# Kernel tuning notes

Measured on AMD Instinct MI355X. Metric: run time of the kernel, lower is better.

Reference implementation:

```python
import jax, jax.numpy as jnp
import numpy as np
from jax import lax

B, S, T = 4096, 4096, 2  # batch, seq_length, num_tags (CRF(2) hardcoded in ToNySegmenter)


def setup_inputs() -> dict:
    key = jax.random.key(0)
    k_em, k_st, k_en, k_tr, k_tg, k_len = jax.random.split(key, 6)
    emissions = jax.random.normal(k_em, (B, S, T), dtype=jnp.float32)
    start_transitions = jax.random.uniform(k_st, (T,), dtype=jnp.float32, minval=-1.0, maxval=1.0)
    end_transitions = jax.random.uniform(k_en, (T,), dtype=jnp.float32, minval=-1.0, maxval=1.0)
    transitions = jax.random.uniform(k_tr, (T, T), dtype=jnp.float32, minval=-1.0, maxval=1.0)
    tags = jax.random.randint(k_tg, (B, S), 0, T, dtype=jnp.int64)
    # variable-length sequences; first position always valid (CRF assumes mask[0]==1)
    lengths = jax.random.randint(k_len, (B,), S // 2, S + 1)
    mask = (jnp.arange(S)[None, :] < lengths[:, None]).astype(jnp.int32)
    return {
        'emissions': emissions,
        'start_transitions': start_transitions,
        'end_transitions': end_transitions,
        'transitions': transitions,
        'tags': tags,
        'mask': mask,
    }


def _crf_nll(emissions, start_transitions, end_transitions, transitions, tags, mask):
    # batch_first=True in the torch module -> transpose to time-major (S, B, ...)
    em = jnp.transpose(emissions, (1, 0, 2))      # (S, B, T)
    tg = tags.T                                   # (S, B)
    mk = mask.T.astype(em.dtype)                  # (S, B)
    seq_len, batch = tg.shape

    # ---- numerator: score of the gold path (fully vectorized over time) ----
    emit = jnp.take_along_axis(em, tg[..., None], axis=2)[..., 0]   # (S, B)
    score = start_transitions[tg[0]] + emit[0]                      # (B,)
    trans = transitions[tg[:-1], tg[1:]]                            # (S-1, B)
    score = score + jnp.sum((trans + emit[1:]) * mk[1:], axis=0)
    seq_ends = mk.sum(axis=0).astype(jnp.int32) - 1                 # (B,)
    last_tags = tg[seq_ends, jnp.arange(batch)]
    score = score + end_transitions[last_tags]

    # ---- denominator: forward algorithm via lax.scan over time ----
    init = start_transitions + em[0]                                # (B, T)

    def step(s, x):
        e_i, m_i = x                                                # (B,T), (B,)
        # s[b, prev] + transitions[prev, cur] + e_i[b, cur], logsumexp over prev
        ns = jax.nn.logsumexp(s[:, :, None] + transitions[None, :, :] + e_i[:, None, :], axis=1)
        s = jnp.where(m_i[:, None] > 0, ns, s)
        return s, None

    final, _ = lax.scan(step, init, (em[1:], mk[1:]))
    normalizer = jax.nn.logsumexp(final + end_transitions, axis=1)  # (B,)

    return -(score - normalizer).mean()


def reference(emissions, start_transitions, end_transitions, transitions, tags, mask):
    return _crf_nll(emissions, start_transitions, end_transitions, transitions, tags, mask)
```

## Files before the change

kernel.cpp:

```cpp
#include <hip/hip_runtime.h>

#define B_CONST 4096
#define S_CONST 4096

#define NEGBIG (-1e30f)

__device__ __forceinline__ float lse2(float a, float b) {
    float m = fmaxf(a, b);
    float d = fminf(a, b) - m;
    return m + __logf(1.0f + __expf(d));
}

struct Seg { float m00, m01, m10, m11; };

__device__ __forceinline__ Seg seg_compose(const Seg& L, const Seg& R) {
    Seg o;
    o.m00 = lse2(L.m00 + R.m00, L.m01 + R.m10);
    o.m01 = lse2(L.m00 + R.m01, L.m01 + R.m11);
    o.m10 = lse2(L.m10 + R.m00, L.m11 + R.m10);
    o.m11 = lse2(L.m10 + R.m01, L.m11 + R.m11);
    return o;
}

__global__ __launch_bounds__(256) void crf_lens_kernel(
    const int* __restrict__ mask, int* __restrict__ lens)
{
    int b = blockIdx.x * 256 + threadIdx.x;
    if (b >= B_CONST) return;
    const int* mk = mask + (size_t)b * S_CONST;
    int lo = 0, hi = S_CONST;
    while (lo < hi) {
        int mid = (lo + hi) >> 1;
        if (mk[mid]) lo = mid + 1; else hi = mid;
    }
    lens[b] = lo;
}

__global__ __launch_bounds__(256) void crf_row_kernel(
    const float* __restrict__ em,
    const float* __restrict__ st,
    const float* __restrict__ en,
    const float* __restrict__ tr,
    const int*   __restrict__ tags,
    const int*   __restrict__ lens,
    float* __restrict__ row_nll)
{
    const int b   = blockIdx.x;
    const int tid = threadIdx.x;
    const float* em_row = em   + (size_t)b * S_CONST * 2;
    const int*   tg_row = tags + (size_t)b * S_CONST;

    const int L = lens[b];

    const float t00 = tr[0], t01 = tr[1], t10 = tr[2], t11 = tr[3];

    const int C  = S_CONST / 256;
    const int c0 = tid * C;
    const int myHi = min(c0 + C, L);

    Seg seg; seg.m00 = 0.0f; seg.m11 = 0.0f; seg.m01 = NEGBIG; seg.m10 = NEGBIG;
    float sc = 0.0f;

    if (c0 < myHi) {
        int prev = (c0 == 0) ? 0 : tg_row[c0 - 1];
        const float4* emv = (const float4*)(em_row + 2 * c0);
        const int4*   tgv = (const int4*)(tg_row + c0);

        #pragma unroll
        for (int k = 0; k < C / 4; ++k) {
            const int tb = c0 + 4 * k;
            if (tb < myHi) {
                int4   tg4 = tgv[k];
                float4 eA  = emv[2 * k];
                float4 eB  = emv[2 * k + 1];

                #define STEP(T_, E0_, E1_, TG_)                                      \
                    do {                                                             \
                        int t_ = (T_);                                               \
                        if (t_ >= 1 && t_ < myHi) {                                  \
                            float e0_ = (E0_), e1_ = (E1_);                          \
                            Seg M;                                                   \
                            M.m00 = t00 + e0_; M.m01 = t01 + e1_;                    \
                            M.m10 = t10 + e0_; M.m11 = t11 + e1_;                    \
                            seg = seg_compose(seg, M);                               \
                            float trv = prev ? ((TG_) ? t11 : t10)                   \
                                             : ((TG_) ? t01 : t00);                  \
                            sc += trv + ((TG_) ? e1_ : e0_);                         \
                        }                                                            \
                        prev = (TG_);                                                \
                    } while (0)

                STEP(tb + 0, eA.x, eA.y, tg4.x);
                STEP(tb + 1, eA.z, eA.w, tg4.y);
                STEP(tb + 2, eB.x, eB.y, tg4.z);
                STEP(tb + 3, eB.z, eB.w, tg4.w);
                #undef STEP
            }
        }
    }

    #pragma unroll
    for (int s = 1; s < 64; s <<= 1) {
        Seg r;
        r.m00 = __shfl_down(seg.m00, s);
        r.m01 = __shfl_down(seg.m01, s);
        r.m10 = __shfl_down(seg.m10, s);
        r.m11 = __shfl_down(seg.m11, s);
        float rsc = __shfl_down(sc, s);
        seg = seg_compose(seg, r);
        sc += rsc;
    }

    __shared__ Seg   wseg[4];
    __shared__ float wsc[4];
    const int lane = tid & 63, wid = tid >> 6;
    if (lane == 0) { wseg[wid] = seg; wsc[wid] = sc; }
    __syncthreads();

    if (tid == 0) {
        Seg P = wseg[0];
        float scT = wsc[0];
        #pragma unroll
        for (int w = 1; w < 4; ++w) { P = seg_compose(P, wseg[w]); scT += wsc[w]; }

        float e00 = em_row[0], e01 = em_row[1];
        float st0 = st[0], st1 = st[1];
        float en0 = en[0], en1 = en[1];

        float i0 = st0 + e00, i1 = st1 + e01;
        float f0 = lse2(i0 + P.m00, i1 + P.m10);
        float f1 = lse2(i0 + P.m01, i1 + P.m11);
        float norm = lse2(f0 + en0, f1 + en1);

        int tg0 = tg_row[0];
        int tgL = tg_row[L - 1];
        float score = (tg0 ? st1 : st0) + (tg0 ? e01 : e00) + scT
                    + (tgL ? en1 : en0);

        row_nll[b] = norm - score;
    }
}

__global__ __launch_bounds__(256) void crf_mean_kernel(
    const float* __restrict__ row_nll, float* __restrict__ out)
{
    float s = 0.0f;
    for (int i = threadIdx.x; i < B_CONST; i += 256) s += row_nll[i];
    #pragma unroll
    for (int d = 32; d >= 1; d >>= 1) s += __shfl_down(s, d);
    __shared__ float ws[4];
    const int lane = threadIdx.x & 63, wid = threadIdx.x >> 6;
    if (lane == 0) ws[wid] = s;
    __syncthreads();
    if (threadIdx.x == 0) {
        out[0] = (ws[0] + ws[1] + ws[2] + ws[3]) / (float)B_CONST;
    }
}

extern "C" void kernel_launch(void* const* d_in, const int* in_sizes, int n_in,
                              void* d_out, int out_size, void* d_ws, size_t ws_size,
                              hipStream_t stream) {
    const float* em   = (const float*)d_in[0];
    const float* st   = (const float*)d_in[1];
    const float* en   = (const float*)d_in[2];
    const float* tr   = (const float*)d_in[3];
    const int*   tags = (const int*)d_in[4];
    const int*   mask = (const int*)d_in[5];

    float* row_nll = (float*)d_ws;
    int*   lens    = (int*)((float*)d_ws + B_CONST);

    float* out = (float*)d_out;

    crf_lens_kernel<<<(B_CONST + 255) / 256, 256, 0, stream>>>(mask, lens);
    crf_row_kernel<<<B_CONST, 256, 0, stream>>>(em, st, en, tr, tags, lens, row_nll);
    crf_mean_kernel<<<1, 256, 0, stream>>>(row_nll, out);
}
```

Before: 318.9 us.

## Use 1024-thread rows, wave-ballot length search, and atomic mean

The row kernel now uses 1024 threads per row with 4 timesteps each instead of 256 threads with 16 each, so more memory parallelism is in flight. The previous tag at chunk boundaries now comes from a lane shuffle. The mask length search becomes a two-level wave ballot with one wave per row, replacing a per-thread binary search. The separate mean kernel is replaced by a memset plus an atomicAdd per row. This adds a 16-wave serial combine, heavier shuffle reductions and 4096 contended atomics, and the float sum order becomes nondeterministic.

```diff
diff --git a/kernel.cpp b/kernel.cpp
--- a/kernel.cpp
+++ b/kernel.cpp
@@ -25,28 +25,34 @@
 __global__ __launch_bounds__(256) void crf_lens_kernel(
     const int* __restrict__ mask, int* __restrict__ lens)
 {
-    int b = blockIdx.x * 256 + threadIdx.x;
+    const int lane = threadIdx.x & 63;
+    const int wid  = threadIdx.x >> 6;
+    const int b    = blockIdx.x * 4 + wid;
     if (b >= B_CONST) return;
     const int* mk = mask + (size_t)b * S_CONST;
-    int lo = 0, hi = S_CONST;
-    while (lo < hi) {
-        int mid = (lo + hi) >> 1;
-        if (mk[mid]) lo = mid + 1; else hi = mid;
-    }
-    lens[b] = lo;
+
+    int v1 = mk[lane * 64];
+    unsigned long long bal1 = __ballot(v1);
+    int nb = __popcll(bal1);
+    int base = (nb - 1) * 64;
+    int v2 = mk[base + lane];
+    unsigned long long bal2 = __ballot(v2);
+    int L = base + __popcll(bal2);
+    if (lane == 0) lens[b] = L;
 }
 
-__global__ __launch_bounds__(256) void crf_row_kernel(
+__global__ __launch_bounds__(1024) void crf_row_kernel(
     const float* __restrict__ em,
     const float* __restrict__ st,
     const float* __restrict__ en,
     const float* __restrict__ tr,
     const int*   __restrict__ tags,
     const int*   __restrict__ lens,
-    float* __restrict__ row_nll)
+    float* __restrict__ out)
 {
     const int b   = blockIdx.x;
     const int tid = threadIdx.x;
+    const int lane = tid & 63, wid = tid >> 6;
     const float* em_row = em   + (size_t)b * S_CONST * 2;
     const int*   tg_row = tags + (size_t)b * S_CONST;
 
@@ -54,49 +60,45 @@
 
     const float t00 = tr[0], t01 = tr[1], t10 = tr[2], t11 = tr[3];
 
-    const int C  = S_CONST / 256;
-    const int c0 = tid * C;
-    const int myHi = min(c0 + C, L);
+    const int c0   = tid * 4;
+    const int myHi = min(c0 + 4, L);
+    const bool active = (c0 < L);
 
     Seg seg; seg.m00 = 0.0f; seg.m11 = 0.0f; seg.m01 = NEGBIG; seg.m10 = NEGBIG;
     float sc = 0.0f;
 
-    if (c0 < myHi) {
-        int prev = (c0 == 0) ? 0 : tg_row[c0 - 1];
+    int4 tg4 = make_int4(0, 0, 0, 0);
+    if (active) tg4 = *(const int4*)(tg_row + c0);
+
+    int prev = __shfl_up(tg4.w, 1);
+    if (lane == 0) prev = (c0 > 0 && active) ? tg_row[c0 - 1] : 0;
+
+    if (active) {
         const float4* emv = (const float4*)(em_row + 2 * c0);
-        const int4*   tgv = (const int4*)(tg_row + c0);
+        float4 eA = emv[0];
+        float4 eB = emv[1];
 
-        #pragma unroll
-        for (int k = 0; k < C / 4; ++k) {
-            const int tb = c0 + 4 * k;
-            if (tb < myHi) {
-                int4   tg4 = tgv[k];
-                float4 eA  = emv[2 * k];
-                float4 eB  = emv[2 * k + 1];
+        #define STEP(T_, E0_, E1_, TG_)                                      \
+            do {                                                             \
+                int t_ = (T_);                                               \
+                if (t_ >= 1 && t_ < myHi) {                                  \
+                    float e0_ = (E0_), e1_ = (E1_);                          \
+                    Seg M;                                                   \
+                    M.m00 = t00 + e0_; M.m01 = t01 + e1_;                    \
+                    M.m10 = t10 + e0_; M.m11 = t11 + e1_;                    \
+                    seg = seg_compose(seg, M);                               \
+                    float trv = prev ? ((TG_) ? t11 : t10)                   \
+                                     : ((TG_) ? t01 : t00);                  \
+                    sc += trv + ((TG_) ? e1_ : e0_);                         \
+                }                                                            \
+                prev = (TG_);                                                \
+            } while (0)
 
-                #define STEP(T_, E0_, E1_, TG_)                                      \
-                    do {                                                             \
-                        int t_ = (T_);                                               \
-                        if (t_ >= 1 && t_ < myHi) {                                  \
-                            float e0_ = (E0_), e1_ = (E1_);                          \
-                            Seg M;                                                   \
-                            M.m00 = t00 + e0_; M.m01 = t01 + e1_;                    \
-                            M.m10 = t10 + e0_; M.m11 = t11 + e1_;                    \
-                            seg = seg_compose(seg, M);                               \
-                            float trv = prev ? ((TG_) ? t11 : t10)                   \
-                                             : ((TG_) ? t01 : t00);                  \
-                            sc += trv + ((TG_) ? e1_ : e0_);                         \
-                        }                                                            \
-                        prev = (TG_);                                                \
-                    } while (0)
-
-                STEP(tb + 0, eA.x, eA.y, tg4.x);
-                STEP(tb + 1, eA.z, eA.w, tg4.y);
-                STEP(tb + 2, eB.x, eB.y, tg4.z);
-                STEP(tb + 3, eB.z, eB.w, tg4.w);
-                #undef STEP
-            }
-        }
+        STEP(c0 + 0, eA.x, eA.y, tg4.x);
+        STEP(c0 + 1, eA.z, eA.w, tg4.y);
+        STEP(c0 + 2, eB.x, eB.y, tg4.z);
+        STEP(c0 + 3, eB.z, eB.w, tg4.w);
+        #undef STEP
     }
 
     #pragma unroll
@@ -111,9 +113,8 @@
         sc += rsc;
     }
 
-    __shared__ Seg   wseg[4];
-    __shared__ float wsc[4];
-    const int lane = tid & 63, wid = tid >> 6;
+    __shared__ Seg   wseg[16];
+    __shared__ float wsc[16];
     if (lane == 0) { wseg[wid] = seg; wsc[wid] = sc; }
     __syncthreads();
 
@@ -121,7 +122,7 @@
         Seg P = wseg[0];
         float scT = wsc[0];
         #pragma unroll
-        for (int w = 1; w < 4; ++w) { P = seg_compose(P, wseg[w]); scT += wsc[w]; }
+        for (int w = 1; w < 16; ++w) { P = seg_compose(P, wseg[w]); scT += wsc[w]; }
 
         float e00 = em_row[0], e01 = em_row[1];
         float st0 = st[0], st1 = st[1];
@@ -137,23 +138,7 @@
         float score = (tg0 ? st1 : st0) + (tg0 ? e01 : e00) + scT
                     + (tgL ? en1 : en0);
 
-        row_nll[b] = norm - score;
-    }
-}
-
-__global__ __launch_bounds__(256) void crf_mean_kernel(
-    const float* __restrict__ row_nll, float* __restrict__ out)
-{
-    float s = 0.0f;
-    for (int i = threadIdx.x; i < B_CONST; i += 256) s += row_nll[i];
-    #pragma unroll
-    for (int d = 32; d >= 1; d >>= 1) s += __shfl_down(s, d);
-    __shared__ float ws[4];
-    const int lane = threadIdx.x & 63, wid = threadIdx.x >> 6;
-    if (lane == 0) ws[wid] = s;
-    __syncthreads();
-    if (threadIdx.x == 0) {
-        out[0] = (ws[0] + ws[1] + ws[2] + ws[3]) / (float)B_CONST;
+        atomicAdd(out, (norm - score) * (1.0f / (float)B_CONST));
     }
 }
 
@@ -167,12 +152,10 @@
     const int*   tags = (const int*)d_in[4];
     const int*   mask = (const int*)d_in[5];
 
-    float* row_nll = (float*)d_ws;
-    int*   lens    = (int*)((float*)d_ws + B_CONST);
+    int*   lens = (int*)d_ws;
+    float* out  = (float*)d_out;
 
-    float* out = (float*)d_out;
-
-    crf_lens_kernel<<<(B_CONST + 255) / 256, 256, 0, stream>>>(mask, lens);
-    crf_row_kernel<<<B_CONST, 256, 0, stream>>>(em, st, en, tr, tags, lens, row_nll);
-    crf_mean_kernel<<<1, 256, 0, stream>>>(row_nll, out);
+    hipMemsetAsync(out, 0, sizeof(float) * out_size, stream);
+    crf_lens_kernel<<<(B_CONST + 3) / 4, 256, 0, stream>>>(mask, lens);
+    crf_row_kernel<<<B_CONST, 1024, 0, stream>>>(em, st, en, tr, tags, lens, out);
 }
```

Result: no change. 324.3 us (+1.7%).
